# Performance work log

Hardware: AMD Instinct MI355X
Metric: run time of the kernel (lower is better)

Reference implementation:

```python
import jax, jax.numpy as jnp
import numpy as np

P = 1024          # nodes per graph
B = 64            # graphs in batch
N = P * B         # total nodes
E = N * 32        # total edges (avg degree 32)
D_IN = 16         # per-node feature dim (share_obs_dim)
H = 32            # GCN / MLP hidden dim (hardcoded in GNet)
SHARE = 64        # flat share_state dim


def setup_inputs() -> dict:
    key = jax.random.key(0)
    ks = jax.random.split(key, 20)

    x = jax.random.normal(ks[0], (N, D_IN), jnp.float32)
    src = jax.random.randint(ks[1], (E,), 0, N, dtype=jnp.int32)
    # keep edges inside each 1024-node graph block (PyG batched graphs)
    dst = (src // P) * P + jax.random.randint(ks[2], (E,), 0, P, dtype=jnp.int32)
    edge_index = jnp.stack([src, dst])
    value_batch = (jnp.arange(N, dtype=jnp.int32) // P)
    share_state = jax.random.normal(ks[3], (B, SHARE), jnp.float32)

    def lin(k, o, i):
        return jax.random.normal(k, (o, i), jnp.float32) / np.float32(np.sqrt(i))

    return {
        "x": x, "edge_index": edge_index, "value_batch": value_batch,
        "share_state": share_state,
        # value_gnet: GCNConv(D_IN,32), GCNConv(32,32), Linear(32,32), post-pool Linear(32,32)
        "W1": lin(ks[4], H, D_IN), "b1": jnp.zeros((H,), jnp.float32),
        "W2": lin(ks[5], H, H),    "b2": jnp.zeros((H,), jnp.float32),
        "Wl": lin(ks[6], H, H),    "bl": jnp.zeros((H,), jnp.float32),
        "Wp": lin(ks[7], H, H),    "bp": jnp.zeros((H,), jnp.float32),
        # value_net MLP: SHARE->32->32->32
        "Vw1": lin(ks[8], H, SHARE), "Vb1": jnp.zeros((H,), jnp.float32),
        "Vw2": lin(ks[9], H, H),     "Vb2": jnp.zeros((H,), jnp.float32),
        "Vw3": lin(ks[10], H, H),    "Vb3": jnp.zeros((H,), jnp.float32),
        # value_comnet: 64->32->1
        "Cw1": lin(ks[11], H, 2 * H), "Cb1": jnp.zeros((H,), jnp.float32),
        "Cw2": lin(ks[12], 1, H) * np.float32(0.01), "Cb2": jnp.zeros((1,), jnp.float32),
    }


def gcn_conv(x, src, dst, W, b):
    """PyG GCNConv: D^-1/2 (A+I) D^-1/2 X W^T + b (unit edge weights)."""
    n = x.shape[0]
    loop = jnp.arange(n, dtype=src.dtype)
    s = jnp.concatenate([src, loop])
    d = jnp.concatenate([dst, loop])
    deg = jax.ops.segment_sum(jnp.ones(s.shape[0], x.dtype), d, num_segments=n)
    dis = jnp.where(deg > 0, jax.lax.rsqrt(jnp.maximum(deg, 1e-12)), 0.0)
    norm = dis[s] * dis[d]                      # [E+N]
    h = x @ W.T                                  # [N, H] small GEMM first
    out = jax.ops.segment_sum(h[s] * norm[:, None], d, num_segments=n)
    return out + b


def reference(x, edge_index, value_batch, share_state,
              W1, b1, W2, b2, Wl, bl, Wp, bp,
              Vw1, Vb1, Vw2, Vb2, Vw3, Vb3,
              Cw1, Cb1, Cw2, Cb2):
    src, dst = edge_index[0], edge_index[1]
    nb = share_state.shape[0]

    # value_gnet
    h = jnp.tanh(gcn_conv(x, src, dst, W1, b1))
    h = jnp.tanh(gcn_conv(h, src, dst, W2, b2))
    h = jnp.tanh(h @ Wl.T + bl)
    pooled = jax.ops.segment_sum(h, value_batch, num_segments=nb)  # global_add_pool -> [B, 32]
    h1 = pooled @ Wp.T + bp

    # value_net MLP on flat share_state
    h2 = jnp.tanh(share_state @ Vw1.T + Vb1)
    h2 = jnp.tanh(h2 @ Vw2.T + Vb2)
    h2 = h2 @ Vw3.T + Vb3

    # value_comnet
    z = jnp.tanh(jnp.concatenate([h1, h2], axis=-1) @ Cw1.T + Cb1)
    value = z @ Cw2.T + Cb2                      # [B, 1]
    return value
```

## Files before the change

### kernel.cpp

```cpp
#include <hip/hip_runtime.h>
#include <math.h>

#define NNODES 65536
#define NEDGES 2097152
#define PGRAPH 1024
#define NGRAPH 64
#define CAPE_E 34560
#define CAPQ   9728
#define CSRG   (4 * CAPQ)

#define OFF_GFILL 0u
#define OFF_POOL4 256u
#define OFF_ROWI  33024u
#define OFF_DIS   295168u
#define OFF_CSR   557312u
#define OFF_EBUF  5538048u
#define OFF_H1    14385408u

__device__ __forceinline__ float ftanh(float x) {
    float e = __expf(2.f * x);
    return 1.f - 2.f * __builtin_amdgcn_rcpf(e + 1.f);
}

__global__ void k_bucket(const int* __restrict__ src, const int* __restrict__ dst,
                         int* __restrict__ gfill, unsigned int* __restrict__ ebuf) {
    __shared__ unsigned int sorted[8192];
    __shared__ int hist[64], lexcl[64], gbase[64], lfill[64];
    int t = threadIdx.x;
    if (t < 64) { hist[t] = 0; lfill[t] = 0; }
    __syncthreads();

    const int4* src4 = (const int4*)(src + blockIdx.x * 8192);
    const int4* dst4 = (const int4*)(dst + blockIdx.x * 8192);
    unsigned int pk[32];
    #pragma unroll
    for (int k = 0; k < 8; k++) {
        int4 s4 = src4[k * 256 + t];
        int4 d4 = dst4[k * 256 + t];
        int ss[4] = { s4.x, s4.y, s4.z, s4.w };
        int dd[4] = { d4.x, d4.y, d4.z, d4.w };
        #pragma unroll
        for (int j = 0; j < 4; j++) {
            int g = ss[j] >> 10;
            pk[k * 4 + j] = (unsigned int)((ss[j] & 1023) | ((dd[j] & 1023) << 10) | (g << 20));
            atomicAdd(&hist[g], 1);
        }
    }
    __syncthreads();
    if (t < 64) {
        int h = hist[t];
        int x = h;
        #pragma unroll
        for (int off = 1; off < 64; off <<= 1) {
            int y = __shfl_up(x, off, 64);
            if (t >= off) x += y;
        }
        lexcl[t] = x - h;
        gbase[t] = atomicAdd(&gfill[t], h);
    }
    __syncthreads();
    #pragma unroll
    for (int k = 0; k < 32; k++) {
        int g = pk[k] >> 20;
        int pos = lexcl[g] + atomicAdd(&lfill[g], 1);
        sorted[pos] = pk[k];
    }
    __syncthreads();
    for (int i = t; i < 8192; i += 256) {
        unsigned int p = sorted[i];
        int g = p >> 20;
        ebuf[(size_t)g * CAPE_E + gbase[g] + (i - lexcl[g])] = p;
    }
}

__global__ __launch_bounds__(1024, 1) void k_build_conv1(
        const float* __restrict__ x, const float* __restrict__ W,
        const float* __restrict__ bias,
        const unsigned int* __restrict__ ebuf, const int* __restrict__ gfill,
        float* __restrict__ disg, unsigned int* __restrict__ rowinfo,
        unsigned short* __restrict__ csr, float* __restrict__ h1) {
    __shared__ float hsL[1025 * 32];
    __shared__ unsigned short lcsr[CAPQ];
    __shared__ int uhist[1024];
    __shared__ int lrow[256], lfill[256];
    __shared__ int wsum[4];
    float4* hsL4 = (float4*)hsL;

    int t = threadIdx.x;
    int g = blockIdx.x >> 2, part = blockIdx.x & 3;
    int cnt = gfill[g];
    const unsigned int* eb = ebuf + (size_t)g * CAPE_E;

    uhist[t] = 0;
    if (t < 32) hsL[1024 * 32 + t] = 0.f;
    __syncthreads();
    for (int i = t; i < cnt; i += 1024) atomicAdd(&uhist[(eb[i] >> 10) & 1023], 1);
    __syncthreads();

    int dv_own = uhist[t];
    float dis_own = rsqrtf((float)(dv_own + 1));

    int dq = 0, r4 = 0;
    if (t < 256) { dq = uhist[part * 256 + t]; r4 = (dq + 3) & ~3; }
    int lane = t & 63, wid = t >> 6;
    int xx = r4;
    #pragma unroll
    for (int off = 1; off < 64; off <<= 1) {
        int y = __shfl_up(xx, off, 64);
        if (lane >= off) xx += y;
    }
    if (t < 256 && lane == 63) wsum[wid] = xx;
    __syncthreads();
    if (t < 256) {
        int pre = 0;
        for (int w = 0; w < wid; w++) pre += wsum[w];
        lrow[t] = pre + xx - r4;
        lfill[t] = 0;
    }
    __syncthreads();

    for (int i = t; i < cnt; i += 1024) {
        unsigned int v = eb[i];
        int d = (v >> 10) & 1023;
        if ((d >> 8) == part) {
            int dl = d & 255;
            int pos = lrow[dl] + atomicAdd(&lfill[dl], 1);
            lcsr[pos] = (unsigned short)(v & 1023);
        }
    }
    __syncthreads();
    if (t < 256) {
        int st = lrow[t];
        for (int i = dq; i < r4; i++) lcsr[st + i] = 1024;
        int n = (g << 10) + part * 256 + t;
        disg[n] = rsqrtf((float)(dq + 1));
        rowinfo[n] = ((unsigned int)st << 16) | (unsigned int)dq;
    }
    __syncthreads();

    int qlen = lrow[255] + ((uhist[part * 256 + 255] + 3) & ~3);
    {
        const ushort4* l4 = (const ushort4*)lcsr;
        ushort4* c4 = (ushort4*)(csr + (size_t)g * CSRG + part * CAPQ);
        for (int i = t; i < (qlen >> 2); i += 1024) c4[i] = l4[i];
    }

    {
        int n = (g << 10) + t;
        float inr[16];
        const float4* in4 = (const float4*)(x + (size_t)n * 16);
        #pragma unroll
        for (int k = 0; k < 4; k++) {
            float4 v = in4[k];
            inr[4*k] = v.x; inr[4*k+1] = v.y; inr[4*k+2] = v.z; inr[4*k+3] = v.w;
        }
        int sw = t & 7;
        #pragma unroll
        for (int o4 = 0; o4 < 8; o4++) {
            float r[4];
            #pragma unroll
            for (int j = 0; j < 4; j++) {
                int o = o4 * 4 + j;
                float s = 0.f;
                #pragma unroll
                for (int k = 0; k < 16; k++) s += inr[k] * W[o * 16 + k];
                r[j] = s * dis_own;
            }
            hsL4[t * 8 + (o4 ^ sw)] = make_float4(r[0], r[1], r[2], r[3]);
        }
    }
    __syncthreads();

    int q = t & 7, grp = t >> 3;
    #pragma unroll
    for (int pass = 0; pass < 2; pass++) {
        int lq = pass * 128 + grp;
        int ln = part * 256 + lq;
        int d = uhist[ln];
        float dn = rsqrtf((float)(d + 1));
        int st = lrow[lq];
        float4 acc = hsL4[ln * 8 + (q ^ (ln & 7))];
        const ushort4* c4 = (const ushort4*)(lcsr + st);
        int d4 = (d + 3) >> 2;
        for (int i = 0; i < d4; i++) {
            ushort4 ss = c4[i];
            float4 v0 = hsL4[ss.x * 8 + (q ^ (ss.x & 7))];
            float4 v1 = hsL4[ss.y * 8 + (q ^ (ss.y & 7))];
            float4 v2 = hsL4[ss.z * 8 + (q ^ (ss.z & 7))];
            float4 v3 = hsL4[ss.w * 8 + (q ^ (ss.w & 7))];
            acc.x += (v0.x + v1.x) + (v2.x + v3.x);
            acc.y += (v0.y + v1.y) + (v2.y + v3.y);
            acc.z += (v0.z + v1.z) + (v2.z + v3.z);
            acc.w += (v0.w + v1.w) + (v2.w + v3.w);
        }
        float4 bb = ((const float4*)bias)[q];
        float4 r;
        r.x = ftanh(dn * acc.x + bb.x);
        r.y = ftanh(dn * acc.y + bb.y);
        r.z = ftanh(dn * acc.z + bb.z);
        r.w = ftanh(dn * acc.w + bb.w);
        ((float4*)h1)[((size_t)(g << 10) + ln) * 8 + q] = r;
    }
}

__global__ __launch_bounds__(1024, 1) void k_conv2(
        const float* __restrict__ h1, const float* __restrict__ W,
        const float* __restrict__ bias, const float* __restrict__ disg,
        const unsigned int* __restrict__ rowinfo, const unsigned short* __restrict__ csr,
        const float* __restrict__ Wl, const float* __restrict__ bl,
        float* __restrict__ pooled4) {
    __shared__ float hsL[1025 * 32];
    __shared__ float WlL[32 * 33];
    float4* hsL4 = (float4*)hsL;

    int t = threadIdx.x;
    int g = blockIdx.x >> 2, part = blockIdx.x & 3;

    if (t < 32 * 32) WlL[(t >> 5) * 33 + (t & 31)] = Wl[t];
    if (t < 32) hsL[1024 * 32 + t] = 0.f;

    {
        int n = (g << 10) + t;
        float inr[32];
        const float4* in4 = (const float4*)(h1 + (size_t)n * 32);
        #pragma unroll
        for (int k = 0; k < 8; k++) {
            float4 v = in4[k];
            inr[4*k] = v.x; inr[4*k+1] = v.y; inr[4*k+2] = v.z; inr[4*k+3] = v.w;
        }
        float dn = disg[n];
        int sw = t & 7;
        #pragma unroll
        for (int o4 = 0; o4 < 8; o4++) {
            float r[4];
            #pragma unroll
            for (int j = 0; j < 4; j++) {
                int o = o4 * 4 + j;
                float s = 0.f;
                #pragma unroll
                for (int k = 0; k < 32; k++) s += inr[k] * W[o * 32 + k];
                r[j] = s * dn;
            }
            hsL4[t * 8 + (o4 ^ sw)] = make_float4(r[0], r[1], r[2], r[3]);
        }
    }
    __syncthreads();

    int q = t & 7, grp = t >> 3;
    float4 racc[2];
    #pragma unroll
    for (int pass = 0; pass < 2; pass++) {
        int lq = pass * 128 + grp;
        int ln = part * 256 + lq;
        int n = (g << 10) + ln;
        unsigned int ri = rowinfo[n];
        int st = ri >> 16;
        int d  = ri & 0xFFFF;
        float dn = rsqrtf((float)(d + 1));
        float4 acc = hsL4[ln * 8 + (q ^ (ln & 7))];
        const ushort4* c4 = (const ushort4*)(csr + (size_t)g * CSRG + part * CAPQ + st);
        int d4 = (d + 3) >> 2;
        for (int i = 0; i < d4; i++) {
            ushort4 ss = c4[i];
            float4 v0 = hsL4[ss.x * 8 + (q ^ (ss.x & 7))];
            float4 v1 = hsL4[ss.y * 8 + (q ^ (ss.y & 7))];
            float4 v2 = hsL4[ss.z * 8 + (q ^ (ss.z & 7))];
            float4 v3 = hsL4[ss.w * 8 + (q ^ (ss.w & 7))];
            acc.x += (v0.x + v1.x) + (v2.x + v3.x);
            acc.y += (v0.y + v1.y) + (v2.y + v3.y);
            acc.z += (v0.z + v1.z) + (v2.z + v3.z);
            acc.w += (v0.w + v1.w) + (v2.w + v3.w);
        }
        float4 bb = ((const float4*)bias)[q];
        float4 r;
        r.x = ftanh(dn * acc.x + bb.x);
        r.y = ftanh(dn * acc.y + bb.y);
        r.z = ftanh(dn * acc.z + bb.z);
        r.w = ftanh(dn * acc.w + bb.w);
        racc[pass] = r;
    }

    __syncthreads();
    #pragma unroll
    for (int pass = 0; pass < 2; pass++) {
        int lnn = pass * 128 + grp;
        hsL4[lnn * 8 + (q ^ (lnn & 7))] = racc[pass];
    }
    __syncthreads();
    int o = t & 31, seg = t >> 5;
    float ps = 0.f;
    #pragma unroll
    for (int j = 0; j < 8; j++) {
        int nl = seg * 8 + j;
        int swn = nl & 7;
        float s = bl[o];
        #pragma unroll
        for (int k = 0; k < 32; k++) {
            float h2v = hsL[nl * 32 + ((((k >> 2) ^ swn) << 2) | (k & 3))];
            s += h2v * WlL[o * 33 + k];
        }
        ps += ftanh(s);
    }
    float* psum = hsL + 8192;
    psum[t] = ps;
    __syncthreads();
    if (t < 32) {
        float tot = 0.f;
        for (int s = 0; s < 32; s++) tot += psum[s * 32 + t];
        pooled4[blockIdx.x * 32 + t] = tot;
    }
}

__global__ void k_final(const float* __restrict__ pooled4, const float* __restrict__ share,
                        const float* __restrict__ Wp,  const float* __restrict__ bp,
                        const float* __restrict__ Vw1, const float* __restrict__ Vb1,
                        const float* __restrict__ Vw2, const float* __restrict__ Vb2,
                        const float* __restrict__ Vw3, const float* __restrict__ Vb3,
                        const float* __restrict__ Cw1, const float* __restrict__ Cb1,
                        const float* __restrict__ Cw2, const float* __restrict__ Cb2,
                        float* __restrict__ out) {
    int id = blockIdx.x * 256 + threadIdx.x;
    int b = id >> 5;
    int j = id & 31;
    float p = pooled4[(b * 4 + 0) * 32 + j] + pooled4[(b * 4 + 1) * 32 + j]
            + pooled4[(b * 4 + 2) * 32 + j] + pooled4[(b * 4 + 3) * 32 + j];
    float h1v = bp[j];
    #pragma unroll
    for (int k = 0; k < 32; k++) h1v += Wp[j * 32 + k] * __shfl(p, k, 32);
    float s0 = share[b * 64 + j];
    float s1 = share[b * 64 + 32 + j];
    float t1 = Vb1[j];
    #pragma unroll
    for (int k = 0; k < 32; k++) {
        t1 += Vw1[j * 64 + k] * __shfl(s0, k, 32);
        t1 += Vw1[j * 64 + 32 + k] * __shfl(s1, k, 32);
    }
    t1 = tanhf(t1);
    float t2 = Vb2[j];
    #pragma unroll
    for (int k = 0; k < 32; k++) t2 += Vw2[j * 32 + k] * __shfl(t1, k, 32);
    t2 = tanhf(t2);
    float h2v = Vb3[j];
    #pragma unroll
    for (int k = 0; k < 32; k++) h2v += Vw3[j * 32 + k] * __shfl(t2, k, 32);
    float z = Cb1[j];
    #pragma unroll
    for (int k = 0; k < 32; k++) {
        z += Cw1[j * 64 + k] * __shfl(h1v, k, 32);
        z += Cw1[j * 64 + 32 + k] * __shfl(h2v, k, 32);
    }
    z = tanhf(z);
    float v = Cw2[j] * z;
    v += __shfl_down(v, 16, 32); v += __shfl_down(v, 8, 32);
    v += __shfl_down(v, 4, 32);  v += __shfl_down(v, 2, 32);
    v += __shfl_down(v, 1, 32);
    if (j == 0) out[b] = v + Cb2[0];
}

extern "C" void kernel_launch(void* const* d_in, const int* in_sizes, int n_in,
                              void* d_out, int out_size, void* d_ws, size_t ws_size,
                              hipStream_t stream) {
    const float* x     = (const float*)d_in[0];
    const int*   ei    = (const int*)d_in[1];
    const float* share = (const float*)d_in[3];
    const float* W1 = (const float*)d_in[4];  const float* b1 = (const float*)d_in[5];
    const float* W2 = (const float*)d_in[6];  const float* b2 = (const float*)d_in[7];
    const float* Wl = (const float*)d_in[8];  const float* bl = (const float*)d_in[9];
    const float* Wp = (const float*)d_in[10]; const float* bp = (const float*)d_in[11];
    const float* Vw1 = (const float*)d_in[12]; const float* Vb1 = (const float*)d_in[13];
    const float* Vw2 = (const float*)d_in[14]; const float* Vb2 = (const float*)d_in[15];
    const float* Vw3 = (const float*)d_in[16]; const float* Vb3 = (const float*)d_in[17];
    const float* Cw1 = (const float*)d_in[18]; const float* Cb1 = (const float*)d_in[19];
    const float* Cw2 = (const float*)d_in[20]; const float* Cb2 = (const float*)d_in[21];

    char* ws = (char*)d_ws;
    int*            gfill   = (int*)(ws + OFF_GFILL);
    float*          pooled4 = (float*)(ws + OFF_POOL4);
    unsigned int*   rowinfo = (unsigned int*)(ws + OFF_ROWI);
    float*          disg    = (float*)(ws + OFF_DIS);
    unsigned short* csr     = (unsigned short*)(ws + OFF_CSR);
    unsigned int*   ebuf    = (unsigned int*)(ws + OFF_EBUF);
    float*          h1      = (float*)(ws + OFF_H1);

    const int* srcp = ei;
    const int* dstp = ei + NEDGES;

    hipMemsetAsync(gfill, 0, 256, stream);

    k_bucket<<<256, 256, 0, stream>>>(srcp, dstp, gfill, ebuf);
    k_build_conv1<<<256, 1024, 0, stream>>>(x, W1, b1, ebuf, gfill,
                                            disg, rowinfo, csr, h1);
    k_conv2<<<256, 1024, 0, stream>>>(h1, W2, b2, disg, rowinfo, csr,
                                      Wl, bl, pooled4);
    k_final<<<8, 256, 0, stream>>>(pooled4, share, Wp, bp, Vw1, Vb1, Vw2, Vb2,
                                   Vw3, Vb3, Cw1, Cb1, Cw2, Cb2, (float*)d_out);
}
```

Baseline: 191.5 us.

## Store intermediate GCN activations as bf16 and hoist feature loads

```diff
diff --git a/kernel.cpp b/kernel.cpp
--- a/kernel.cpp
+++ b/kernel.cpp
@@ -22,6 +22,18 @@
     return 1.f - 2.f * __builtin_amdgcn_rcpf(e + 1.f);
 }
 
+__device__ __forceinline__ unsigned short pack_bf16(float f) {
+    unsigned int b = __float_as_uint(f);
+    b += 0x7FFFu + ((b >> 16) & 1u);
+    return (unsigned short)(b >> 16);
+}
+__device__ __forceinline__ float unpack_bf16_lo(unsigned int u) {
+    return __uint_as_float(u << 16);
+}
+__device__ __forceinline__ float unpack_bf16_hi(unsigned int u) {
+    return __uint_as_float(u & 0xFFFF0000u);
+}
+
 __global__ void k_bucket(const int* __restrict__ src, const int* __restrict__ dst,
                          int* __restrict__ gfill, unsigned int* __restrict__ ebuf) {
     __shared__ unsigned int sorted[8192];
@@ -78,7 +90,7 @@
         const float* __restrict__ bias,
         const unsigned int* __restrict__ ebuf, const int* __restrict__ gfill,
         float* __restrict__ disg, unsigned int* __restrict__ rowinfo,
-        unsigned short* __restrict__ csr, float* __restrict__ h1) {
+        unsigned short* __restrict__ csr, unsigned short* __restrict__ h1) {
     __shared__ float hsL[1025 * 32];
     __shared__ unsigned short lcsr[CAPQ];
     __shared__ int uhist[1024];
@@ -87,9 +99,19 @@
     float4* hsL4 = (float4*)hsL;
 
     int t = threadIdx.x;
-    int g = blockIdx.x >> 2, part = blockIdx.x & 3;
+    int g = blockIdx.x & 63, part = blockIdx.x >> 6;
     int cnt = gfill[g];
     const unsigned int* eb = ebuf + (size_t)g * CAPE_E;
+
+    float inr[16];
+    {
+        const float4* in4 = (const float4*)(x + ((size_t)(g << 10) + t) * 16);
+        #pragma unroll
+        for (int k = 0; k < 4; k++) {
+            float4 v = in4[k];
+            inr[4*k] = v.x; inr[4*k+1] = v.y; inr[4*k+2] = v.z; inr[4*k+3] = v.w;
+        }
+    }
 
     uhist[t] = 0;
     if (t < 32) hsL[1024 * 32 + t] = 0.f;
@@ -146,14 +168,6 @@
     }
 
     {
-        int n = (g << 10) + t;
-        float inr[16];
-        const float4* in4 = (const float4*)(x + (size_t)n * 16);
-        #pragma unroll
-        for (int k = 0; k < 4; k++) {
-            float4 v = in4[k];
-            inr[4*k] = v.x; inr[4*k+1] = v.y; inr[4*k+2] = v.z; inr[4*k+3] = v.w;
-        }
         int sw = t & 7;
         #pragma unroll
         for (int o4 = 0; o4 < 8; o4++) {
@@ -194,17 +208,17 @@
             acc.w += (v0.w + v1.w) + (v2.w + v3.w);
         }
         float4 bb = ((const float4*)bias)[q];
-        float4 r;
-        r.x = ftanh(dn * acc.x + bb.x);
-        r.y = ftanh(dn * acc.y + bb.y);
-        r.z = ftanh(dn * acc.z + bb.z);
-        r.w = ftanh(dn * acc.w + bb.w);
-        ((float4*)h1)[((size_t)(g << 10) + ln) * 8 + q] = r;
+        ushort4 r;
+        r.x = pack_bf16(ftanh(dn * acc.x + bb.x));
+        r.y = pack_bf16(ftanh(dn * acc.y + bb.y));
+        r.z = pack_bf16(ftanh(dn * acc.z + bb.z));
+        r.w = pack_bf16(ftanh(dn * acc.w + bb.w));
+        ((ushort4*)h1)[((size_t)(g << 10) + ln) * 8 + q] = r;
     }
 }
 
 __global__ __launch_bounds__(1024, 1) void k_conv2(
-        const float* __restrict__ h1, const float* __restrict__ W,
+        const unsigned short* __restrict__ h1, const float* __restrict__ W,
         const float* __restrict__ bias, const float* __restrict__ disg,
         const unsigned int* __restrict__ rowinfo, const unsigned short* __restrict__ csr,
         const float* __restrict__ Wl, const float* __restrict__ bl,
@@ -214,21 +228,29 @@
     float4* hsL4 = (float4*)hsL;
 
     int t = threadIdx.x;
-    int g = blockIdx.x >> 2, part = blockIdx.x & 3;
+    int g = blockIdx.x & 63, part = blockIdx.x >> 6;
+
+    float inr[32];
+    {
+        const uint4* in4 = (const uint4*)(h1 + ((size_t)(g << 10) + t) * 32);
+        #pragma unroll
+        for (int k = 0; k < 4; k++) {
+            uint4 v = in4[k];
+            unsigned int uu[4] = { v.x, v.y, v.z, v.w };
+            #pragma unroll
+            for (int j = 0; j < 4; j++) {
+                inr[8*k + 2*j]     = unpack_bf16_lo(uu[j]);
+                inr[8*k + 2*j + 1] = unpack_bf16_hi(uu[j]);
+            }
+        }
+    }
+    float dn_own = disg[(g << 10) + t];
 
     if (t < 32 * 32) WlL[(t >> 5) * 33 + (t & 31)] = Wl[t];
     if (t < 32) hsL[1024 * 32 + t] = 0.f;
+    __syncthreads();
 
     {
-        int n = (g << 10) + t;
-        float inr[32];
-        const float4* in4 = (const float4*)(h1 + (size_t)n * 32);
-        #pragma unroll
-        for (int k = 0; k < 8; k++) {
-            float4 v = in4[k];
-            inr[4*k] = v.x; inr[4*k+1] = v.y; inr[4*k+2] = v.z; inr[4*k+3] = v.w;
-        }
-        float dn = disg[n];
         int sw = t & 7;
         #pragma unroll
         for (int o4 = 0; o4 < 8; o4++) {
@@ -239,7 +261,7 @@
                 float s = 0.f;
                 #pragma unroll
                 for (int k = 0; k < 32; k++) s += inr[k] * W[o * 32 + k];
-                r[j] = s * dn;
+                r[j] = s * dn_own;
             }
             hsL4[t * 8 + (o4 ^ sw)] = make_float4(r[0], r[1], r[2], r[3]);
         }
@@ -307,7 +329,7 @@
     if (t < 32) {
         float tot = 0.f;
         for (int s = 0; s < 32; s++) tot += psum[s * 32 + t];
-        pooled4[blockIdx.x * 32 + t] = tot;
+        pooled4[(g * 4 + part) * 32 + t] = tot;
     }
 }
 
@@ -380,7 +402,7 @@
     float*          disg    = (float*)(ws + OFF_DIS);
     unsigned short* csr     = (unsigned short*)(ws + OFF_CSR);
     unsigned int*   ebuf    = (unsigned int*)(ws + OFF_EBUF);
-    float*          h1      = (float*)(ws + OFF_H1);
+    unsigned short* h1      = (unsigned short*)(ws + OFF_H1);
 
     const int* srcp = ei;
     const int* dstp = ei + NEDGES;
```

Result: faster. 186.7 us (-2.5%).
